# Kernel optimization log

Measured on AMD Instinct MI355X. Metric: run time of the kernel, lower is better.

Reference implementation:

```python
import jax, jax.numpy as jnp
import numpy as np

N = 50000   # nodes
E = 800000  # edges (before self-loops)
IN = 256    # in_dim
H = 4       # heads
C = 64      # out_dim per head
NEG_SLOPE = 0.2
BN_EPS = 1e-5


def setup_inputs() -> dict:
    key = jax.random.key(0)
    ks = jax.random.split(key, 6)
    feature = jax.random.normal(ks[0], (N, IN), jnp.float32)
    edge_index = jax.random.randint(ks[1], (2, E), 0, N, dtype=jnp.int64)
    W = jax.random.normal(ks[2], (IN, H * C), jnp.float32) * 0.05
    att_src = jax.random.normal(ks[3], (H, C), jnp.float32) * 0.1
    att_dst = jax.random.normal(ks[4], (H, C), jnp.float32) * 0.1
    bias = jnp.zeros((H * C,), jnp.float32)
    gamma = jnp.ones((H * C,), jnp.float32)
    beta = jnp.zeros((H * C,), jnp.float32)
    return {"feature": feature, "edge_index": edge_index, "W": W,
            "att_src": att_src, "att_dst": att_dst, "bias": bias,
            "gamma": gamma, "beta": beta}


def reference(feature, edge_index, W, att_src, att_dst, bias, gamma, beta):
    n = feature.shape[0]
    # linear projection -> [N, H, C]
    x = (feature @ W).reshape(n, H, C)
    # per-node attention logits [N, H]
    a_src = jnp.einsum('nhc,hc->nh', x, att_src)
    a_dst = jnp.einsum('nhc,hc->nh', x, att_dst)
    # add self loops (PyG GATConv default)
    loop = jnp.arange(n, dtype=edge_index.dtype)
    src = jnp.concatenate([edge_index[0], loop])
    dst = jnp.concatenate([edge_index[1], loop])
    # edge attention scores [E+N, H]
    e = jax.nn.leaky_relu(a_src[src] + a_dst[dst], NEG_SLOPE)
    # segment softmax over incoming edges of each dst node
    m = jax.ops.segment_max(e, dst, num_segments=n)
    ex = jnp.exp(e - m[dst])
    denom = jax.ops.segment_sum(ex, dst, num_segments=n)
    alpha = ex / denom[dst]                       # [E+N, H]
    # weighted message aggregation -> [N, H, C]
    msg = x[src] * alpha[:, :, None]
    out = jax.ops.segment_sum(msg, dst, num_segments=n)
    h = out.reshape(n, H * C) + bias
    # batchnorm over nodes (training-mode batch statistics)
    mu = jnp.mean(h, axis=0)
    var = jnp.var(h, axis=0)
    h = (h - mu) * jax.lax.rsqrt(var + BN_EPS) * gamma + beta
    # ELU activation
    h = jax.nn.elu(h)
    # residual (in_dim == out_dim * num_heads)
    return feature + h
```

## Files before the change

kernel.cpp:

```cpp
#include <hip/hip_runtime.h>

#define N_NODES 50000
#define N_EDGES 800000
#define NEG_SLOPE 0.2f
#define BN_EPS  1e-5f

#define CHUNKS 256
#define EDGES_PER_CHUNK 3125
#define NCOARSE 1024
#define NBUCKET 782

typedef short bf16x8 __attribute__((ext_vector_type(8)));
typedef float floatx4 __attribute__((ext_vector_type(4)));

__device__ inline ushort f2bf(float f) {
    union { float f; unsigned u; } v; v.f = f;
    unsigned r = v.u + 0x7fff + ((v.u >> 16) & 1);
    return (ushort)(r >> 16);
}
__device__ inline float bf2f(ushort h) {
    union { unsigned u; float f; } v; v.u = ((unsigned)h) << 16;
    return v.f;
}

__global__ __launch_bounds__(256) void count_wt_kernel(const int* __restrict__ ei,
                                                       const float* __restrict__ W,
                                                       int* __restrict__ counts,
                                                       ushort* __restrict__ Wtb)
{
    __shared__ int hist[NCOARSE];
    const int t = threadIdx.x;
    const int b = blockIdx.x;
    if (b < CHUNKS) {
        for (int j = t; j < NCOARSE; j += 256) hist[j] = 0;
        __syncthreads();
        const int e0 = b * EDGES_PER_CHUNK;
        for (int e = e0 + t; e < e0 + EDGES_PER_CHUNK; e += 256)
            atomicAdd(&hist[ei[N_EDGES + e] >> 6], 1);
        __syncthreads();
        for (int j = t; j < NCOARSE; j += 256)
            counts[j * CHUNKS + b] = hist[j];
    } else {
        const int n = b - CHUNKS;
        Wtb[n * 256 + t] = f2bf(W[t * 256 + n]);
    }
}

__global__ __launch_bounds__(256) void sscan1_kernel(int* __restrict__ counts,
                                                     int* __restrict__ blocksum)
{
    __shared__ int sm[256];
    const int t = threadIdx.x;
    const int i = blockIdx.x * 256 + t;
    const int v = counts[i];
    sm[t] = v;
    __syncthreads();
#pragma unroll
    for (int off = 1; off < 256; off <<= 1) {
        const int u = (t >= off) ? sm[t - off] : 0;
        __syncthreads();
        sm[t] += u;
        __syncthreads();
    }
    counts[i] = sm[t] - v;
    if (t == 255) blocksum[blockIdx.x] = sm[255];
}

__global__ __launch_bounds__(256) void sscan2_kernel(const int* __restrict__ blocksum,
                                                     int* __restrict__ blockbase,
                                                     float* __restrict__ gsum,
                                                     float* __restrict__ gsumsq)
{
    __shared__ int sm[256];
    const int t = threadIdx.x;
    int v[4], loc[4], tot = 0;
#pragma unroll
    for (int j = 0; j < 4; ++j) {
        v[j] = blocksum[t * 4 + j];
        loc[j] = tot;
        tot += v[j];
    }
    sm[t] = tot;
    __syncthreads();
#pragma unroll
    for (int off = 1; off < 256; off <<= 1) {
        const int u = (t >= off) ? sm[t - off] : 0;
        __syncthreads();
        sm[t] += u;
        __syncthreads();
    }
    const int base = sm[t] - tot;
#pragma unroll
    for (int j = 0; j < 4; ++j) blockbase[t * 4 + j] = base + loc[j];
    gsum[t] = 0.f;
    gsumsq[t] = 0.f;
}

__global__ __launch_bounds__(256) void bucket_scatter_kernel(const int* __restrict__ ei,
                                                             const int* __restrict__ counts,
                                                             const int* __restrict__ blockbase,
                                                             uint* __restrict__ tmp)
{
    __shared__ int cursor[NCOARSE];
    const int t = threadIdx.x;
    const int blk = blockIdx.x;
    for (int u = t; u < NCOARSE; u += 256)
        cursor[u] = counts[u * CHUNKS + blk] + blockbase[u];
    __syncthreads();
    const int e0 = blk * EDGES_PER_CHUNK;
    for (int e = e0 + t; e < e0 + EDGES_PER_CHUNK; e += 256) {
        const int src = ei[e];
        const int dst = ei[N_EDGES + e];
        const int pos = atomicAdd(&cursor[dst >> 6], 1);
        tmp[pos] = ((uint)src << 6) | (uint)(dst & 63);
    }
}

__global__ __launch_bounds__(256) void bucket_build_kernel(const uint* __restrict__ tmp,
                                                           const int* __restrict__ blockbase,
                                                           int* __restrict__ offsets,
                                                           int* __restrict__ csr_src)
{
    __shared__ int hist[64];
    __shared__ int sbuf[64];
    __shared__ int cursor[64];
    const int t = threadIdx.x;
    const int b = blockIdx.x;
    const int start = blockbase[b];
    const int end   = blockbase[b + 1];
    if (t < 64) hist[t] = 0;
    __syncthreads();
    for (int e = start + t; e < end; e += 256)
        atomicAdd(&hist[tmp[e] & 63], 1);
    __syncthreads();
    const int v = (t < 64) ? hist[t] : 0;
    if (t < 64) sbuf[t] = v;
    __syncthreads();
#pragma unroll
    for (int off = 1; off < 64; off <<= 1) {
        int u = 0;
        if (t < 64 && t >= off) u = sbuf[t - off];
        __syncthreads();
        if (t < 64) sbuf[t] += u;
        __syncthreads();
    }
    if (t < 64) {
        const int excl = start + sbuf[t] - v;
        cursor[t] = excl;
        const int node = b * 64 + t;
        if (node < N_NODES) offsets[node] = excl;
    }
    if (b == 0 && t == 0) offsets[N_NODES] = N_EDGES;
    __syncthreads();
    for (int e = start + t; e < end; e += 256) {
        const uint p = tmp[e];
        const int pos = atomicAdd(&cursor[p & 63], 1);
        csr_src[pos] = (int)(p >> 6);
    }
}

#define LDSTRIDE 40
__global__ __launch_bounds__(256) void gemm_kernel(const float* __restrict__ A,
                                                   const ushort* __restrict__ Bt,
                                                   const float* __restrict__ att_src,
                                                   const float* __restrict__ att_dst,
                                                   ushort* __restrict__ Xb,
                                                   float* __restrict__ s,
                                                   float* __restrict__ d)
{
    __shared__ ushort As[128 * LDSTRIDE];
    __shared__ ushort Bs[128 * LDSTRIDE];
    const int tid = threadIdx.x;
    const int lane = tid & 63;
    const int wid = tid >> 6;
    const int wm = wid & 1, wn = wid >> 1;
    const int row0 = blockIdx.y * 128;
    const int col0 = blockIdx.x * 128;

    floatx4 acc[4][4] = {};

    const int lr = tid >> 2;
    const int lk = (tid & 3) * 8;

    for (int k0 = 0; k0 < 256; k0 += 32) {
#pragma unroll
        for (int r = 0; r < 2; ++r) {
            const int row = lr + r * 64;
            const int grow = row0 + row;
            union { ushort u[8]; ulonglong2 v; } cv;
            if (grow < N_NODES) {
                const float4 f0 = *(const float4*)(A + (size_t)grow * 256 + k0 + lk);
                const float4 f1 = *(const float4*)(A + (size_t)grow * 256 + k0 + lk + 4);
                cv.u[0] = f2bf(f0.x); cv.u[1] = f2bf(f0.y);
                cv.u[2] = f2bf(f0.z); cv.u[3] = f2bf(f0.w);
                cv.u[4] = f2bf(f1.x); cv.u[5] = f2bf(f1.y);
                cv.u[6] = f2bf(f1.z); cv.u[7] = f2bf(f1.w);
            } else {
                cv.v = ulonglong2{0ull, 0ull};
            }
            *(ulonglong2*)(As + row * LDSTRIDE + lk) = cv.v;
            const ulonglong2 bv = *(const ulonglong2*)(Bt + (size_t)(col0 + row) * 256 + k0 + lk);
            *(ulonglong2*)(Bs + row * LDSTRIDE + lk) = bv;
        }
        __syncthreads();
        const int quad = lane >> 4;
        const int l16 = lane & 15;
        bf16x8 afrag[4], bfrag[4];
#pragma unroll
        for (int mi = 0; mi < 4; ++mi)
            afrag[mi] = *(const bf16x8*)(As + (wm * 64 + mi * 16 + l16) * LDSTRIDE + quad * 8);
#pragma unroll
        for (int ni = 0; ni < 4; ++ni)
            bfrag[ni] = *(const bf16x8*)(Bs + (wn * 64 + ni * 16 + l16) * LDSTRIDE + quad * 8);
#pragma unroll
        for (int mi = 0; mi < 4; ++mi)
#pragma unroll
            for (int ni = 0; ni < 4; ++ni)
                acc[mi][ni] = __builtin_amdgcn_mfma_f32_16x16x32_bf16(afrag[mi], bfrag[ni], acc[mi][ni], 0, 0, 0);
        __syncthreads();
    }

    const int quad = lane >> 4;
    const int l16 = lane & 15;
    const int head = (col0 + wn * 64) >> 6;
    float as_l[4], ad_l[4];
#pragma unroll
    for (int ni = 0; ni < 4; ++ni) {
        const int ch = head * 64 + ni * 16 + l16;
        as_l[ni] = att_src[ch];
        ad_l[ni] = att_dst[ch];
    }
#pragma unroll
    for (int mi = 0; mi < 4; ++mi) {
#pragma unroll
        for (int r = 0; r < 4; ++r) {
            const int grow = row0 + wm * 64 + mi * 16 + quad * 4 + r;
            const bool ok = grow < N_NODES;
            float vs = 0.f, vd = 0.f;
            ushort4 o;
#pragma unroll
            for (int ni = 0; ni < 4; ++ni) {
                const float v = acc[mi][ni][r];
                vs += v * as_l[ni];
                vd += v * ad_l[ni];
                ((ushort*)&o)[ni] = f2bf(v);
            }
            if (ok)
                *(ushort4*)(Xb + (size_t)grow * 256 + head * 64 + l16 * 4) = o;
#pragma unroll
            for (int m = 8; m >= 1; m >>= 1) {
                vs += __shfl_xor(vs, m);
                vd += __shfl_xor(vd, m);
            }
            if (l16 == 0 && ok) {
                s[grow * 4 + head] = vs;
                d[grow * 4 + head] = vd;
            }
        }
    }
}

__global__ __launch_bounds__(256) void aggregate_kernel(const ushort* __restrict__ xb,
                                                        const float* __restrict__ s,
                                                        const float* __restrict__ d,
                                                        const int* __restrict__ offsets,
                                                        const int* __restrict__ csr_src,
                                                        ushort* __restrict__ hagg)
{
    const int wid = threadIdx.x >> 6;
    const int lane = threadIdx.x & 63;
    const int n = blockIdx.x * 4 + wid;
    if (n >= N_NODES) return;
    const int h = lane >> 4;
    const float dn = d[n * 4 + h];
    const float sn = s[n * 4 + h];
    const ushort4 xr = *(const ushort4*)(xb + (size_t)n * 256 + lane * 4);
    float eself = sn + dn;
    eself = eself >= 0.f ? eself : NEG_SLOPE * eself;
    const float pself = __expf(eself);
    float den = pself;
    float a0 = pself * bf2f(xr.x), a1 = pself * bf2f(xr.y);
    float a2 = pself * bf2f(xr.z), a3 = pself * bf2f(xr.w);
    const int e0 = offsets[n];
    const int e1 = offsets[n + 1];
    int e = e0;
    for (; e + 8 <= e1; e += 8) {
        int si[8];
        float lg[8];
        ushort4 xv[8];
#pragma unroll
        for (int j = 0; j < 8; ++j) si[j] = csr_src[e + j];
#pragma unroll
        for (int j = 0; j < 8; ++j) lg[j] = s[si[j] * 4 + h] + dn;
#pragma unroll
        for (int j = 0; j < 8; ++j)
            xv[j] = *(const ushort4*)(xb + (size_t)si[j] * 256 + lane * 4);
#pragma unroll
        for (int j = 0; j < 8; ++j) {
            float l = lg[j];
            l = l >= 0.f ? l : NEG_SLOPE * l;
            const float p = __expf(l);
            den += p;
            a0 += p * bf2f(xv[j].x);
            a1 += p * bf2f(xv[j].y);
            a2 += p * bf2f(xv[j].z);
            a3 += p * bf2f(xv[j].w);
        }
    }
    for (; e < e1; ++e) {
        const int src = csr_src[e];
        float ee = s[src * 4 + h] + dn;
        ee = ee >= 0.f ? ee : NEG_SLOPE * ee;
        const float pe = __expf(ee);
        const ushort4 xs = *(const ushort4*)(xb + (size_t)src * 256 + lane * 4);
        a0 += pe * bf2f(xs.x); a1 += pe * bf2f(xs.y);
        a2 += pe * bf2f(xs.z); a3 += pe * bf2f(xs.w);
        den += pe;
    }
    const float inv = 1.0f / den;
    ushort4 o;
    o.x = f2bf(a0 * inv); o.y = f2bf(a1 * inv);
    o.z = f2bf(a2 * inv); o.w = f2bf(a3 * inv);
    *(ushort4*)(hagg + (size_t)n * 256 + lane * 4) = o;
}

#define BN_BLOCKS 784
__global__ __launch_bounds__(256) void bn_stats_kernel(const ushort* __restrict__ hagg,
                                                       float* __restrict__ gsum,
                                                       float* __restrict__ gsumsq)
{
    const int c = threadIdx.x;
    const int r0 = blockIdx.x * 64;
    float sum = 0.f, sq = 0.f;
#pragma unroll 4
    for (int i = 0; i < 64; ++i) {
        const int r = r0 + i;
        if (r < N_NODES) {
            const float v = bf2f(hagg[(size_t)r * 256 + c]);
            sum += v;
            sq += v * v;
        }
    }
    atomicAdd(&gsum[c], sum);
    atomicAdd(&gsumsq[c], sq);
}

__global__ __launch_bounds__(256) void finalize_kernel(const float* __restrict__ feature,
                                                       const ushort* __restrict__ hagg,
                                                       const float* __restrict__ gsum,
                                                       const float* __restrict__ gsumsq,
                                                       const float* __restrict__ gamma,
                                                       const float* __restrict__ beta,
                                                       float* __restrict__ out)
{
    const int wid = threadIdx.x >> 6;
    const int lane = threadIdx.x & 63;
    const int wgid = blockIdx.x * 4 + wid;
    const int hblk = lane >> 4;
    const int l16 = lane & 15;

    float meanv[4], scalev[4], betav[4];
    int tc[4];
#pragma unroll
    for (int j = 0; j < 4; ++j) {
        const int p = lane * 4 + j;
        tc[j] = hblk * 64 + j * 16 + l16;
        const float m = gsum[p] * (1.0f / N_NODES);
        const float var = gsumsq[p] * (1.0f / N_NODES) - m * m;
        meanv[j] = m;
        scalev[j] = gamma[tc[j]] * rsqrtf(var + BN_EPS);
        betav[j] = beta[tc[j]];
    }
#pragma unroll
    for (int rr = 0; rr < 4; ++rr) {
        const int n = wgid * 4 + rr;
        const ushort4 hv = *(const ushort4*)(hagg + (size_t)n * 256 + lane * 4);
        const float hvf[4] = {bf2f(hv.x), bf2f(hv.y), bf2f(hv.z), bf2f(hv.w)};
#pragma unroll
        for (int j = 0; j < 4; ++j) {
            float r = (hvf[j] - meanv[j]) * scalev[j] + betav[j];
            r = r > 0.f ? r : expm1f(r);
            out[(size_t)n * 256 + tc[j]] = r + feature[(size_t)n * 256 + tc[j]];
        }
    }
}

extern "C" void kernel_launch(void* const* d_in, const int* in_sizes, int n_in,
                              void* d_out, int out_size, void* d_ws, size_t ws_size,
                              hipStream_t stream)
{
    const float* feature = (const float*)d_in[0];
    const int*   ei      = (const int*)d_in[1];
    const float* W       = (const float*)d_in[2];
    const float* att_src = (const float*)d_in[3];
    const float* att_dst = (const float*)d_in[4];
    const float* gamma   = (const float*)d_in[6];
    const float* beta    = (const float*)d_in[7];
    float* out = (float*)d_out;

    char* w = (char*)d_ws;
    auto carve = [&](size_t bytes) {
        char* p = w;
        w += (bytes + 255) & ~(size_t)255;
        return p;
    };
    ushort* Wtb      = (ushort*)carve((size_t)256 * 256 * 2);
    ushort* xb       = (ushort*)carve((size_t)N_NODES * 256 * 2);
    ushort* hagg     = (ushort*)carve((size_t)N_NODES * 256 * 2);
    float*  s        = (float*)carve((size_t)N_NODES * 4 * 4);
    float*  dv       = (float*)carve((size_t)N_NODES * 4 * 4);
    int*    counts   = (int*)carve((size_t)NCOARSE * CHUNKS * 4);
    int*    offsets  = (int*)carve((size_t)(N_NODES + 1) * 4);
    int*    csr_src  = (int*)carve((size_t)N_EDGES * 4);
    int*    blocksum = (int*)carve((size_t)NCOARSE * 4);
    int*    blockbase= (int*)carve((size_t)NCOARSE * 4);
    float*  gsum     = (float*)carve(256 * 4);
    float*  gsumsq   = (float*)carve(256 * 4);
    uint*   tmp      = (uint*)hagg;

    count_wt_kernel<<<512, 256, 0, stream>>>(ei, W, counts, Wtb);
    sscan1_kernel<<<NCOARSE, 256, 0, stream>>>(counts, blocksum);
    sscan2_kernel<<<1, 256, 0, stream>>>(blocksum, blockbase, gsum, gsumsq);
    bucket_scatter_kernel<<<CHUNKS, 256, 0, stream>>>(ei, counts, blockbase, tmp);
    bucket_build_kernel<<<NBUCKET, 256, 0, stream>>>(tmp, blockbase, offsets, csr_src);
    gemm_kernel<<<dim3(2, 391), 256, 0, stream>>>(feature, Wtb, att_src, att_dst, xb, s, dv);
    aggregate_kernel<<<12500, 256, 0, stream>>>(xb, s, dv, offsets, csr_src, hagg);
    bn_stats_kernel<<<BN_BLOCKS, 256, 0, stream>>>(hagg, gsum, gsumsq);
    finalize_kernel<<<3125, 256, 0, stream>>>(feature, hagg, gsum, gsumsq, gamma, beta, out);
}
```

Measured before the change: 291.8 us.

## Fuse scan into scatter, retile GEMM to full-width rows, vectorize finalize, use exp2

Folds the single-block second scan into every bucket_scatter block, which removes one kernel launch at the cost of redundant scan work per block. The GEMM now gives each block 64 rows times all 256 columns, so the fp32 feature tile is read and converted to bf16 once instead of twice. Attention logits are prescaled by log2(e) so the aggregation can use exp2f, and CSR indices and offsets are made wave-uniform with readfirstlane. Finalize stages h in LDS to permute columns so the feature read and output write become float4 vectorized.

After: 274.9 us. -5.8%, faster.

```diff
diff --git a/kernel.cpp b/kernel.cpp
--- a/kernel.cpp
+++ b/kernel.cpp
@@ -4,6 +4,7 @@
 #define N_EDGES 800000
 #define NEG_SLOPE 0.2f
 #define BN_EPS  1e-5f
+#define LOG2E   1.44269504088896f
 
 #define CHUNKS 256
 #define EDGES_PER_CHUNK 3125
@@ -26,7 +27,9 @@
 __global__ __launch_bounds__(256) void count_wt_kernel(const int* __restrict__ ei,
                                                        const float* __restrict__ W,
                                                        int* __restrict__ counts,
-                                                       ushort* __restrict__ Wtb)
+                                                       ushort* __restrict__ Wtb,
+                                                       float* __restrict__ gsum,
+                                                       float* __restrict__ gsumsq)
 {
     __shared__ int hist[NCOARSE];
     const int t = threadIdx.x;
@@ -43,6 +46,7 @@
     } else {
         const int n = b - CHUNKS;
         Wtb[n * 256 + t] = f2bf(W[t * 256 + n]);
+        if (n == 0) { gsum[t] = 0.f; gsumsq[t] = 0.f; }
     }
 }
 
@@ -66,13 +70,18 @@
     if (t == 255) blocksum[blockIdx.x] = sm[255];
 }
 
-__global__ __launch_bounds__(256) void sscan2_kernel(const int* __restrict__ blocksum,
-                                                     int* __restrict__ blockbase,
-                                                     float* __restrict__ gsum,
-                                                     float* __restrict__ gsumsq)
+__global__ __launch_bounds__(256) void bucket_scatter_kernel(const int* __restrict__ ei,
+                                                             const int* __restrict__ counts,
+                                                             const int* __restrict__ blocksum,
+                                                             int* __restrict__ blockbase,
+                                                             uint* __restrict__ tmp)
 {
     __shared__ int sm[256];
+    __shared__ int bbase[NCOARSE];
+    __shared__ int cursor[NCOARSE];
     const int t = threadIdx.x;
+    const int blk = blockIdx.x;
+
     int v[4], loc[4], tot = 0;
 #pragma unroll
     for (int j = 0; j < 4; ++j) {
@@ -91,21 +100,15 @@
     }
     const int base = sm[t] - tot;
 #pragma unroll
-    for (int j = 0; j < 4; ++j) blockbase[t * 4 + j] = base + loc[j];
-    gsum[t] = 0.f;
-    gsumsq[t] = 0.f;
-}
-
-__global__ __launch_bounds__(256) void bucket_scatter_kernel(const int* __restrict__ ei,
-                                                             const int* __restrict__ counts,
-                                                             const int* __restrict__ blockbase,
-                                                             uint* __restrict__ tmp)
-{
-    __shared__ int cursor[NCOARSE];
-    const int t = threadIdx.x;
-    const int blk = blockIdx.x;
+    for (int j = 0; j < 4; ++j) bbase[t * 4 + j] = base + loc[j];
+    if (blk == 0) {
+#pragma unroll
+        for (int j = 0; j < 4; ++j) blockbase[t * 4 + j] = base + loc[j];
+    }
+    __syncthreads();
+
     for (int u = t; u < NCOARSE; u += 256)
-        cursor[u] = counts[u * CHUNKS + blk] + blockbase[u];
+        cursor[u] = counts[u * CHUNKS + blk] + bbase[u];
     __syncthreads();
     const int e0 = blk * EDGES_PER_CHUNK;
     for (int e = e0 + t; e < e0 + EDGES_PER_CHUNK; e += 256) {
@@ -168,14 +171,14 @@
                                                    float* __restrict__ s,
                                                    float* __restrict__ d)
 {
-    __shared__ ushort As[128 * LDSTRIDE];
-    __shared__ ushort Bs[128 * LDSTRIDE];
+    __shared__ ushort As[64 * LDSTRIDE];
+    __shared__ ushort Bs[256 * LDSTRIDE];
     const int tid = threadIdx.x;
     const int lane = tid & 63;
     const int wid = tid >> 6;
-    const int wm = wid & 1, wn = wid >> 1;
-    const int row0 = blockIdx.y * 128;
-    const int col0 = blockIdx.x * 128;
+    const int row0 = blockIdx.x * 64;
+    const int quad = lane >> 4;
+    const int l16  = lane & 15;
 
     floatx4 acc[4][4] = {};
 
@@ -183,10 +186,8 @@
     const int lk = (tid & 3) * 8;
 
     for (int k0 = 0; k0 < 256; k0 += 32) {
-#pragma unroll
-        for (int r = 0; r < 2; ++r) {
-            const int row = lr + r * 64;
-            const int grow = row0 + row;
+        {
+            const int grow = row0 + lr;
             union { ushort u[8]; ulonglong2 v; } cv;
             if (grow < N_NODES) {
                 const float4 f0 = *(const float4*)(A + (size_t)grow * 256 + k0 + lk);
@@ -198,20 +199,22 @@
             } else {
                 cv.v = ulonglong2{0ull, 0ull};
             }
-            *(ulonglong2*)(As + row * LDSTRIDE + lk) = cv.v;
-            const ulonglong2 bv = *(const ulonglong2*)(Bt + (size_t)(col0 + row) * 256 + k0 + lk);
+            *(ulonglong2*)(As + lr * LDSTRIDE + lk) = cv.v;
+        }
+#pragma unroll
+        for (int r = 0; r < 4; ++r) {
+            const int row = lr + r * 64;
+            const ulonglong2 bv = *(const ulonglong2*)(Bt + (size_t)row * 256 + k0 + lk);
             *(ulonglong2*)(Bs + row * LDSTRIDE + lk) = bv;
         }
         __syncthreads();
-        const int quad = lane >> 4;
-        const int l16 = lane & 15;
         bf16x8 afrag[4], bfrag[4];
 #pragma unroll
         for (int mi = 0; mi < 4; ++mi)
-            afrag[mi] = *(const bf16x8*)(As + (wm * 64 + mi * 16 + l16) * LDSTRIDE + quad * 8);
+            afrag[mi] = *(const bf16x8*)(As + (mi * 16 + l16) * LDSTRIDE + quad * 8);
 #pragma unroll
         for (int ni = 0; ni < 4; ++ni)
-            bfrag[ni] = *(const bf16x8*)(Bs + (wn * 64 + ni * 16 + l16) * LDSTRIDE + quad * 8);
+            bfrag[ni] = *(const bf16x8*)(Bs + (wid * 64 + ni * 16 + l16) * LDSTRIDE + quad * 8);
 #pragma unroll
         for (int mi = 0; mi < 4; ++mi)
 #pragma unroll
@@ -220,9 +223,7 @@
         __syncthreads();
     }
 
-    const int quad = lane >> 4;
-    const int l16 = lane & 15;
-    const int head = (col0 + wn * 64) >> 6;
+    const int head = wid;
     float as_l[4], ad_l[4];
 #pragma unroll
     for (int ni = 0; ni < 4; ++ni) {
@@ -234,7 +235,7 @@
     for (int mi = 0; mi < 4; ++mi) {
 #pragma unroll
         for (int r = 0; r < 4; ++r) {
-            const int grow = row0 + wm * 64 + mi * 16 + quad * 4 + r;
+            const int grow = row0 + mi * 16 + quad * 4 + r;
             const bool ok = grow < N_NODES;
             float vs = 0.f, vd = 0.f;
             ushort4 o;
@@ -253,8 +254,8 @@
                 vd += __shfl_xor(vd, m);
             }
             if (l16 == 0 && ok) {
-                s[grow * 4 + head] = vs;
-                d[grow * 4 + head] = vd;
+                s[grow * 4 + head] = vs * LOG2E;
+                d[grow * 4 + head] = vd * LOG2E;
             }
         }
     }
@@ -277,19 +278,19 @@
     const ushort4 xr = *(const ushort4*)(xb + (size_t)n * 256 + lane * 4);
     float eself = sn + dn;
     eself = eself >= 0.f ? eself : NEG_SLOPE * eself;
-    const float pself = __expf(eself);
+    const float pself = exp2f(eself);
     float den = pself;
     float a0 = pself * bf2f(xr.x), a1 = pself * bf2f(xr.y);
     float a2 = pself * bf2f(xr.z), a3 = pself * bf2f(xr.w);
-    const int e0 = offsets[n];
-    const int e1 = offsets[n + 1];
+    const int e0 = __builtin_amdgcn_readfirstlane(offsets[n]);
+    const int e1 = __builtin_amdgcn_readfirstlane(offsets[n + 1]);
     int e = e0;
     for (; e + 8 <= e1; e += 8) {
         int si[8];
         float lg[8];
         ushort4 xv[8];
 #pragma unroll
-        for (int j = 0; j < 8; ++j) si[j] = csr_src[e + j];
+        for (int j = 0; j < 8; ++j) si[j] = __builtin_amdgcn_readfirstlane(csr_src[e + j]);
 #pragma unroll
         for (int j = 0; j < 8; ++j) lg[j] = s[si[j] * 4 + h] + dn;
 #pragma unroll
@@ -299,7 +300,7 @@
         for (int j = 0; j < 8; ++j) {
             float l = lg[j];
             l = l >= 0.f ? l : NEG_SLOPE * l;
-            const float p = __expf(l);
+            const float p = exp2f(l);
             den += p;
             a0 += p * bf2f(xv[j].x);
             a1 += p * bf2f(xv[j].y);
@@ -308,10 +309,10 @@
         }
     }
     for (; e < e1; ++e) {
-        const int src = csr_src[e];
+        const int src = __builtin_amdgcn_readfirstlane(csr_src[e]);
         float ee = s[src * 4 + h] + dn;
         ee = ee >= 0.f ? ee : NEG_SLOPE * ee;
-        const float pe = __expf(ee);
+        const float pe = exp2f(ee);
         const ushort4 xs = *(const ushort4*)(xb + (size_t)src * 256 + lane * 4);
         a0 += pe * bf2f(xs.x); a1 += pe * bf2f(xs.y);
         a2 += pe * bf2f(xs.z); a3 += pe * bf2f(xs.w);
@@ -353,35 +354,56 @@
                                                        const float* __restrict__ beta,
                                                        float* __restrict__ out)
 {
-    const int wid = threadIdx.x >> 6;
-    const int lane = threadIdx.x & 63;
-    const int wgid = blockIdx.x * 4 + wid;
+    __shared__ ushort hs[16][264];
+    const int t = threadIdx.x;
+    const int wid = t >> 6;
+    const int lane = t & 63;
+    const int row0 = blockIdx.x * 16;
     const int hblk = lane >> 4;
     const int l16 = lane & 15;
 
+#pragma unroll
+    for (int rr = 0; rr < 4; ++rr) {
+        const int r = wid * 4 + rr;
+        const int n = row0 + r;
+        const ushort4 hv = *(const ushort4*)(hagg + (size_t)n * 256 + lane * 4);
+        hs[r][hblk * 64 + 0 * 16 + l16] = hv.x;
+        hs[r][hblk * 64 + 1 * 16 + l16] = hv.y;
+        hs[r][hblk * 64 + 2 * 16 + l16] = hv.z;
+        hs[r][hblk * 64 + 3 * 16 + l16] = hv.w;
+    }
+
     float meanv[4], scalev[4], betav[4];
-    int tc[4];
 #pragma unroll
     for (int j = 0; j < 4; ++j) {
-        const int p = lane * 4 + j;
-        tc[j] = hblk * 64 + j * 16 + l16;
+        const int tc = lane * 4 + j;
+        const int w = tc & 63;
+        const int p = (tc >> 6) * 64 + ((w & 15) << 2) + (w >> 4);
         const float m = gsum[p] * (1.0f / N_NODES);
         const float var = gsumsq[p] * (1.0f / N_NODES) - m * m;
         meanv[j] = m;
-        scalev[j] = gamma[tc[j]] * rsqrtf(var + BN_EPS);
-        betav[j] = beta[tc[j]];
-    }
+        scalev[j] = gamma[tc] * rsqrtf(var + BN_EPS);
+        betav[j] = beta[tc];
+    }
+    __syncthreads();
+
 #pragma unroll
     for (int rr = 0; rr < 4; ++rr) {
-        const int n = wgid * 4 + rr;
-        const ushort4 hv = *(const ushort4*)(hagg + (size_t)n * 256 + lane * 4);
+        const int r = wid * 4 + rr;
+        const int n = row0 + r;
+        const ushort4 hv = *(const ushort4*)(&hs[r][lane * 4]);
+        const float4 fv = *(const float4*)(feature + (size_t)n * 256 + lane * 4);
         const float hvf[4] = {bf2f(hv.x), bf2f(hv.y), bf2f(hv.z), bf2f(hv.w)};
+        float4 o;
+        float* op = (float*)&o;
+        const float* fp = (const float*)&fv;
 #pragma unroll
         for (int j = 0; j < 4; ++j) {
-            float r = (hvf[j] - meanv[j]) * scalev[j] + betav[j];
-            r = r > 0.f ? r : expm1f(r);
-            out[(size_t)n * 256 + tc[j]] = r + feature[(size_t)n * 256 + tc[j]];
-        }
+            float v = (hvf[j] - meanv[j]) * scalev[j] + betav[j];
+            v = v > 0.f ? v : expm1f(v);
+            op[j] = v + fp[j];
+        }
+        *(float4*)(out + (size_t)n * 256 + lane * 4) = o;
     }
 }
 
@@ -418,12 +440,11 @@
     float*  gsumsq   = (float*)carve(256 * 4);
     uint*   tmp      = (uint*)hagg;
 
-    count_wt_kernel<<<512, 256, 0, stream>>>(ei, W, counts, Wtb);
+    count_wt_kernel<<<512, 256, 0, stream>>>(ei, W, counts, Wtb, gsum, gsumsq);
     sscan1_kernel<<<NCOARSE, 256, 0, stream>>>(counts, blocksum);
-    sscan2_kernel<<<1, 256, 0, stream>>>(blocksum, blockbase, gsum, gsumsq);
-    bucket_scatter_kernel<<<CHUNKS, 256, 0, stream>>>(ei, counts, blockbase, tmp);
+    bucket_scatter_kernel<<<CHUNKS, 256, 0, stream>>>(ei, counts, blocksum, blockbase, tmp);
     bucket_build_kernel<<<NBUCKET, 256, 0, stream>>>(tmp, blockbase, offsets, csr_src);
-    gemm_kernel<<<dim3(2, 391), 256, 0, stream>>>(feature, Wtb, att_src, att_dst, xb, s, dv);
+    gemm_kernel<<<782, 256, 0, stream>>>(feature, Wtb, att_src, att_dst, xb, s, dv);
     aggregate_kernel<<<12500, 256, 0, stream>>>(xb, s, dv, offsets, csr_src, hagg);
     bn_stats_kernel<<<BN_BLOCKS, 256, 0, stream>>>(hagg, gsum, gsumsq);
     finalize_kernel<<<3125, 256, 0, stream>>>(feature, hagg, gsum, gsumsq, gamma, beta, out);
```
